# Kernel tuning notes

Hardware: AMD Instinct MI355X
Metric: run time of the kernel (lower is better)

## Reference

```python
import jax, jax.numpy as jnp
import numpy as np

N_STREAMS = 4
N_HEADS = 4
D_STATE = 64
EPS_RMS = float(np.finfo(np.float32).eps)


def rms_norm(x, w):
    v = jnp.mean(x * x, axis=-1, keepdims=True)
    return x * jax.lax.rsqrt(v + EPS_RMS) * w


def sinkhorn_mix(logits, iters=5):
    n = logits.shape[0]
    M = jax.nn.sigmoid(logits) + jnp.eye(n, dtype=logits.dtype)
    for _ in range(iters):
        M = M / (M.sum(axis=1, keepdims=True) + 1e-6)
        M = M / (M.sum(axis=0, keepdims=True) + 1e-6)
    return M


def mamba_block(u, norm_w, Wi, bi, A_log, D, dt_bias, Wo, bo):
    B, L, d_model = u.shape
    d_in = 2 * d_model
    P = d_in // N_HEADS
    un = rms_norm(u, norm_w)
    zxbcdt = un @ Wi + bi  # [B,L,4612]
    z = zxbcdt[:, :, :d_in]
    x = zxbcdt[:, :, d_in:2 * d_in].reshape(B, L, N_HEADS, P)
    dt = zxbcdt[:, :, 2 * d_in:2 * d_in + N_HEADS]
    BC = zxbcdt[:, :, 2 * d_in + N_HEADS:].reshape(B, L, N_HEADS, 2, D_STATE)
    B_mat, C_mat = BC[:, :, :, 0], BC[:, :, :, 1]
    dt = jax.nn.softplus(dt + dt_bias)            # [B,L,H]
    A = -jnp.exp(A_log)                            # [H]
    dtA = jnp.exp(dt * A)                          # [B,L,H]
    dtB = dt[..., None] * B_mat                    # [B,L,H,N]

    # time-major scan over the selective-state recurrence
    def step(h, inp):
        dtA_t, dtB_t, x_t, C_t = inp               # [B,H],[B,H,N],[B,H,P],[B,H,N]
        h = h * dtA_t[:, :, None, None] + dtB_t[..., None] * x_t[:, :, None, :]
        y_t = jnp.einsum('bhn,bhnp->bhp', C_t, h)
        return h, y_t

    h0 = jnp.zeros((B, N_HEADS, D_STATE, P), dtype=u.dtype)
    xs = (jnp.moveaxis(dtA, 1, 0), jnp.moveaxis(dtB, 1, 0),
          jnp.moveaxis(x, 1, 0), jnp.moveaxis(C_mat, 1, 0))
    _, ys = jax.lax.scan(step, h0, xs)             # ys: [L,B,H,P]
    y = jnp.moveaxis(ys, 0, 1)                     # [B,L,H,P]
    y = y + x * D[None, None, :, None]
    y = y.reshape(B, L, d_in) * jax.nn.silu(z)
    return y @ Wo + bo


def setup_inputs() -> dict:
    key = jax.random.key(0)
    ks = jax.random.split(key, 10)
    B, L, d_model, vocab, n_layers = 2, 2048, 1024, 32000, 4
    d_proj_out = 2 * 2 * d_model + 2 * N_HEADS * D_STATE + N_HEADS  # 4612
    d_in = 2 * d_model
    s = lambda f: 1.0 / np.sqrt(f)
    return {
        'tokens': jax.random.randint(ks[0], (B, L), 0, vocab, dtype=jnp.int32),
        'embed': jax.random.normal(ks[1], (vocab, d_model), jnp.float32) * 0.02,
        'norm_w': jnp.ones((n_layers, d_model), jnp.float32),
        'in_proj_W': jax.random.normal(ks[2], (n_layers, d_model, d_proj_out), jnp.float32) * s(d_model),
        'in_proj_b': jnp.zeros((n_layers, d_proj_out), jnp.float32),
        'A_log': jnp.full((n_layers, N_HEADS), -4.0, jnp.float32),
        'D': jnp.ones((n_layers, N_HEADS), jnp.float32),
        'dt_bias': jax.random.uniform(ks[3], (n_layers, N_HEADS), jnp.float32) - 4.0,
        'out_proj_W': jax.random.normal(ks[4], (n_layers, d_in, d_model), jnp.float32) * s(d_in),
        'out_proj_b': jnp.zeros((n_layers, d_model), jnp.float32),
        'mixer_logits': jax.random.normal(ks[5], (n_layers, N_STREAMS, N_STREAMS), jnp.float32) * 0.1,
        'norm_f_w': jnp.ones((d_model,), jnp.float32),
        'head_W': jax.random.normal(ks[6], (d_model, vocab), jnp.float32) * s(d_model),
        'head_b': jnp.zeros((vocab,), jnp.float32),
    }


def reference(tokens, embed, norm_w, in_proj_W, in_proj_b, A_log, D, dt_bias,
              out_proj_W, out_proj_b, mixer_logits, norm_f_w, head_W, head_b):
    B, L = tokens.shape
    d_model = embed.shape[1]
    d_sub = d_model // N_STREAMS
    x = embed[tokens]                              # [B,L,d_model]
    H = x.reshape(B, L, N_STREAMS, d_sub)
    n_layers = norm_w.shape[0]
    for l in range(n_layers):
        M = sinkhorn_mix(mixer_logits[l])
        H_res = jnp.einsum('bsid,ji->bsjd', H, M)
        x_out = mamba_block(H.reshape(B, L, d_model), norm_w[l], in_proj_W[l],
                            in_proj_b[l], A_log[l], D[l], dt_bias[l],
                            out_proj_W[l], out_proj_b[l])
        H = H_res + x_out.reshape(B, L, N_STREAMS, d_sub)
    out = rms_norm(H.reshape(B, L, d_model), norm_f_w)
    return out @ head_W + head_b
```

## Files before the change

kernel.cpp:

```cpp
#include <hip/hip_runtime.h>
#include <hip/hip_fp16.h>
#include <cstdint>


typedef _Float16 f16;
typedef __attribute__((ext_vector_type(8))) _Float16 f16x8;
typedef __attribute__((ext_vector_type(4))) _Float16 f16x4;
typedef __attribute__((ext_vector_type(4))) float f32x4;

#define LDS_CAST(p) ((__attribute__((address_space(3))) void*)(p))
#define GLB_CAST(p) ((const __attribute__((address_space(1))) void*)(p))

static __device__ __forceinline__ void gload16(const void* g, void* l) {
    __builtin_amdgcn_global_load_lds(GLB_CAST(g), LDS_CAST(l), 16, 0, 0);
}

__global__ __launch_bounds__(256) void gemm_f16(
    const f16* __restrict__ A, const f16* __restrict__ Bt,
    const float* __restrict__ bias, float* __restrict__ C,
    int M, int N, int K)
{
    __shared__ f16 As[128 * 32];
    __shared__ f16 Bs[128 * 32];
    const int t = threadIdx.x;
    const int lane = t & 63;
    const int w = t >> 6;

    const int gx = gridDim.x;
    const int gy = gridDim.y;
    const int nwg = gx * gy;
    int lin = blockIdx.y * gx + blockIdx.x;
    int xcd = lin & 7, loc = lin >> 3;
    int q = nwg >> 3, rr = nwg & 7;
    int wg = (xcd < rr) ? (xcd * (q + 1) + loc)
                        : (rr * (q + 1) + (xcd - rr) * q + loc);
    const int GROUP = 8;
    int per_group = GROUP * gy;
    int gid = wg / per_group;
    int first_m = gid * GROUP;
    int gsz = (gx - first_m < GROUP) ? (gx - first_m) : GROUP;
    int inner = wg - gid * per_group;
    const int m0 = (first_m + inner % gsz) * 128;
    const int n0 = (inner / gsz) * 128;

    const int wm0 = (w >> 1) * 64, wn0 = (w & 1) * 64;
    const int mrow = lane & 15, ksel = lane >> 4;

    f32x4 zero = {0.f, 0.f, 0.f, 0.f};
    f32x4 acc[4][4];
#pragma unroll
    for (int i = 0; i < 4; i++)
#pragma unroll
        for (int j = 0; j < 4; j++) acc[i][j] = zero;

    const f16* Abase = A + (size_t)m0 * K;
    const f16* Bbase = Bt + (size_t)n0 * K;

    for (int k0 = 0; k0 < K; k0 += 32) {
#pragma unroll
        for (int i = 0; i < 2; i++) {
            int lin2 = t + i * 256;
            int r = lin2 >> 2;
            int cc = (lin2 & 3) * 8;
            gload16(Abase + (size_t)r * K + k0 + cc, As + lin2 * 8);
            gload16(Bbase + (size_t)r * K + k0 + cc, Bs + lin2 * 8);
        }
        __syncthreads();
        f16x8 af[4], bf[4];
#pragma unroll
        for (int i = 0; i < 4; i++) {
            af[i] = *(const f16x8*)(As + (wm0 + i * 16 + mrow) * 32 + ksel * 8);
            bf[i] = *(const f16x8*)(Bs + (wn0 + i * 16 + mrow) * 32 + ksel * 8);
        }
#pragma unroll
        for (int i = 0; i < 4; i++)
#pragma unroll
            for (int j = 0; j < 4; j++)
                acc[i][j] = __builtin_amdgcn_mfma_f32_16x16x32_f16(bf[j], af[i], acc[i][j], 0, 0, 0);
        __syncthreads();
    }

#pragma unroll
    for (int i = 0; i < 4; i++) {
        int m = m0 + wm0 + i * 16 + mrow;
#pragma unroll
        for (int j = 0; j < 4; j++) {
            int nb = n0 + wn0 + j * 16 + ksel * 4;
            if (nb < N) {
                float4 bv = {0.f, 0.f, 0.f, 0.f};
                if (bias) bv = *(const float4*)(bias + nb);
                float4 v;
                v.x = acc[i][j][0] + bv.x;
                v.y = acc[i][j][1] + bv.y;
                v.z = acc[i][j][2] + bv.z;
                v.w = acc[i][j][3] + bv.w;
                *(float4*)(C + (size_t)m * N + nb) = v;
            }
        }
    }
}

__global__ __launch_bounds__(256) void transpose_w(
    const float* __restrict__ W, f16* __restrict__ Wt, int K, int N, int Npad)
{
    __shared__ float tile[32][33];
    int n0 = blockIdx.x * 32, k0 = blockIdx.y * 32;
    int tx = threadIdx.x & 31, ty = threadIdx.x >> 5;
#pragma unroll
    for (int i = 0; i < 4; i++) {
        int k = k0 + ty + 8 * i;
        int n = n0 + tx;
        tile[ty + 8 * i][tx] = (n < N) ? W[(size_t)k * N + n] : 0.f;
    }
    __syncthreads();
#pragma unroll
    for (int i = 0; i < 4; i++) {
        int n = n0 + ty + 8 * i;
        if (n < Npad) Wt[(size_t)n * K + k0 + tx] = (f16)tile[tx][ty + 8 * i];
    }
}

__global__ void sinkhorn_k(const float* __restrict__ logits, float* __restrict__ Mout)
{
    if (threadIdx.x != 0 || blockIdx.x != 0) return;
    for (int l = 0; l < 4; l++) {
        float M[16];
        for (int i = 0; i < 16; i++) {
            float v = logits[l * 16 + i];
            M[i] = 1.f / (1.f + __expf(-v)) + ((i % 5) == 0 ? 1.f : 0.f);
        }
        for (int it = 0; it < 5; it++) {
            for (int r = 0; r < 4; r++) {
                float s = M[r*4] + M[r*4+1] + M[r*4+2] + M[r*4+3] + 1e-6f;
                for (int c = 0; c < 4; c++) M[r*4+c] /= s;
            }
            for (int c = 0; c < 4; c++) {
                float s = M[c] + M[4+c] + M[8+c] + M[12+c] + 1e-6f;
                for (int r = 0; r < 4; r++) M[r*4+c] /= s;
            }
        }
        for (int i = 0; i < 16; i++) Mout[l * 16 + i] = M[i];
    }
}

__global__ __launch_bounds__(256) void embed_gather(
    const int* __restrict__ tokens, const float* __restrict__ embed, float* __restrict__ H)
{
    int i = blockIdx.x * 256 + threadIdx.x;
    int tok = i >> 8, d4 = i & 255;
    int tk = tokens[tok];
    float4 v = ((const float4*)(embed + (size_t)tk * 1024))[d4];
    ((float4*)(H + (size_t)tok * 1024))[d4] = v;
}

__global__ __launch_bounds__(256) void rmsnorm_k(
    const float* __restrict__ X, const float* __restrict__ w, f16* __restrict__ out)
{
    int tok = blockIdx.x;
    int t = threadIdx.x;
    const float4 v = ((const float4*)(X + (size_t)tok * 1024))[t];
    float ss = v.x*v.x + v.y*v.y + v.z*v.z + v.w*v.w;
#pragma unroll
    for (int off = 32; off > 0; off >>= 1) ss += __shfl_down(ss, off, 64);
    __shared__ float wsum[4];
    if ((t & 63) == 0) wsum[t >> 6] = ss;
    __syncthreads();
    float tot = wsum[0] + wsum[1] + wsum[2] + wsum[3];
    float sc = rsqrtf(tot * (1.f / 1024.f) + 1.1920929e-07f);
    const float4 wv = ((const float4*)w)[t];
    f16x4 o;
    o[0] = (f16)(v.x * sc * wv.x);
    o[1] = (f16)(v.y * sc * wv.y);
    o[2] = (f16)(v.z * sc * wv.z);
    o[3] = (f16)(v.w * sc * wv.w);
    ((f16x4*)(out + (size_t)tok * 1024))[t] = o;
}

__global__ __launch_bounds__(256) void dt_cumsum(
    const float* __restrict__ zx, const float* __restrict__ dt_bias,
    const float* __restrict__ A_log,
    float* __restrict__ dt, float* __restrict__ cum, float* __restrict__ E)
{
    int bh = blockIdx.x;
    int b = bh >> 2, h = bh & 3;
    int t = threadIdx.x;
    float Ah = -__expf(A_log[h]);
    float bias = dt_bias[h];
    float run = 0.f, vals[8];
    for (int i = 0; i < 8; i++) {
        int l = t * 8 + i;
        float raw = zx[((size_t)(b * 2048 + l)) * 4612 + 4096 + h] + bias;
        float dtv = (raw > 20.f) ? raw : log1pf(__expf(raw));
        dt[bh * 2048 + l] = dtv;
        run += dtv * Ah;
        vals[i] = run;
    }
    __shared__ float ps[256];
    ps[t] = run;
    __syncthreads();
    for (int off = 1; off < 256; off <<= 1) {
        float v = (t >= off) ? ps[t - off] : 0.f;
        __syncthreads();
        ps[t] += v;
        __syncthreads();
    }
    float offset = (t > 0) ? ps[t - 1] : 0.f;
    for (int i = 0; i < 8; i++) {
        int l = t * 8 + i;
        float cv = vals[i] + offset;
        cum[bh * 2048 + l] = cv;
        if ((l & 63) == 63) E[bh * 32 + (l >> 6)] = cv;
    }
}

__global__ __launch_bounds__(256) void make_xT(
    const float* __restrict__ zx, f16* __restrict__ xT)
{
    int lb = blockIdx.x * 64, pb = blockIdx.y * 64, bh = blockIdx.z;
    int b = bh >> 2, h = bh & 3;
    __shared__ float tile[64][65];
    int tx = threadIdx.x & 63, ty = threadIdx.x >> 6;
#pragma unroll
    for (int i = 0; i < 16; i++) {
        int ll = ty + 4 * i;
        tile[ll][tx] = zx[((size_t)(b * 2048 + lb + ll)) * 4612 + 2048 + h * 512 + pb + tx];
    }
    __syncthreads();
#pragma unroll
    for (int i = 0; i < 16; i++) {
        int pl = ty + 4 * i;
        xT[((size_t)bh * 512 + pb + pl) * 2048 + lb + tx] = (f16)tile[tx][pl];
    }
}

__global__ __launch_bounds__(256) void make_BC(
    const float* __restrict__ zx, f16* __restrict__ Bc, f16* __restrict__ Cc)
{
    int i = blockIdx.x * 256 + threadIdx.x;
    int n = i & 63, h = (i >> 6) & 3, l = (i >> 8) & 2047, b = i >> 19;
    size_t rowoff = ((size_t)(b * 2048 + l)) * 4612 + 4100 + h * 128;
    size_t o = (((size_t)(b * 4 + h)) * 2048 + l) * 64 + n;
    Bc[o] = (f16)zx[rowoff + n];
    Cc[o] = (f16)zx[rowoff + 64 + n];
}

__global__ __launch_bounds__(256) void chunk_intra(
    const f16* __restrict__ Bc, const f16* __restrict__ Cc,
    const f16* __restrict__ xT,
    const float* __restrict__ dt, const float* __restrict__ cum,
    float* __restrict__ Y, float* __restrict__ Hloc)
{
    int c = blockIdx.x, bh = blockIdx.y;
    int l0 = c * 64;
    __shared__ f16 Cs[4096], Bs2[4096], Sb[4096], Wb[4096];
    __shared__ float cums[64], dts[64];
    int t = threadIdx.x;
    {
        const f16x8* sC = (const f16x8*)(Cc + ((size_t)bh * 2048 + l0) * 64);
        const f16x8* sB = (const f16x8*)(Bc + ((size_t)bh * 2048 + l0) * 64);
        ((f16x8*)Cs)[t] = sC[t];
        ((f16x8*)Cs)[t + 256] = sC[t + 256];
        ((f16x8*)Bs2)[t] = sB[t];
        ((f16x8*)Bs2)[t + 256] = sB[t + 256];
    }
    if (t < 64) {
        cums[t] = cum[bh * 2048 + l0 + t];
        dts[t] = dt[bh * 2048 + l0 + t];
    }
    __syncthreads();
    float cumEnd = cums[63];
    int lane = t & 63, w = t >> 6;
    int mrow = lane & 15, ksel = lane >> 4;

    {
        f16x8 cf[2];
        cf[0] = *(const f16x8*)(Cs + (w * 16 + mrow) * 64 + ksel * 8);
        cf[1] = *(const f16x8*)(Cs + (w * 16 + mrow) * 64 + 32 + ksel * 8);
#pragma unroll
        for (int j = 0; j < 4; j++) {
            f32x4 d = {0.f, 0.f, 0.f, 0.f};
#pragma unroll
            for (int ks = 0; ks < 2; ks++) {
                f16x8 bfv = *(const f16x8*)(Bs2 + (j * 16 + mrow) * 64 + ks * 32 + ksel * 8);
                d = __builtin_amdgcn_mfma_f32_16x16x32_f16(cf[ks], bfv, d, 0, 0, 0);
            }
            int ss = j * 16 + mrow;
#pragma unroll
            for (int r = 0; r < 4; r++) {
                int tt = w * 16 + ksel * 4 + r;
                float sv = (ss <= tt) ? d[r] * __expf(cums[tt] - cums[ss]) * dts[ss] : 0.f;
                Sb[tt * 64 + ss] = (f16)sv;
            }
        }
#pragma unroll
        for (int q2 = 0; q2 < 16; q2++) {
            int idx = t * 16 + q2;
            int tt = idx >> 6, ss = idx & 63;
            float wv = (float)Bs2[ss * 64 + tt] * __expf(cumEnd - cums[ss]) * dts[ss];
            Wb[tt * 64 + ss] = (f16)wv;
        }
    }
    __syncthreads();

    f16x8 sfr[2][4], wfr[2][4];
#pragma unroll
    for (int ks = 0; ks < 2; ks++)
#pragma unroll
        for (int mt = 0; mt < 4; mt++) {
            sfr[ks][mt] = *(const f16x8*)(Sb + (mt * 16 + mrow) * 64 + ks * 32 + ksel * 8);
            wfr[ks][mt] = *(const f16x8*)(Wb + (mt * 16 + mrow) * 64 + ks * 32 + ksel * 8);
        }
    const f16* xbase = xT + ((size_t)bh * 512) * 2048 + c * 64;
    f32x4 zero = {0.f, 0.f, 0.f, 0.f};
#pragma unroll
    for (int ph = 0; ph < 2; ph++) {
        int pb = w * 128 + ph * 64;
        f32x4 aY[4][4], aH[4][4];
#pragma unroll
        for (int i = 0; i < 4; i++)
#pragma unroll
            for (int j = 0; j < 4; j++) { aY[i][j] = zero; aH[i][j] = zero; }
#pragma unroll
        for (int ks = 0; ks < 2; ks++) {
#pragma unroll
            for (int nt = 0; nt < 4; nt++) {
                int pp = pb + nt * 16 + mrow;
                f16x8 bfv = *(const f16x8*)(xbase + (size_t)pp * 2048 + ks * 32 + ksel * 8);
#pragma unroll
                for (int mt = 0; mt < 4; mt++) {
                    aY[mt][nt] = __builtin_amdgcn_mfma_f32_16x16x32_f16(sfr[ks][mt], bfv, aY[mt][nt], 0, 0, 0);
                    aH[mt][nt] = __builtin_amdgcn_mfma_f32_16x16x32_f16(wfr[ks][mt], bfv, aH[mt][nt], 0, 0, 0);
                }
            }
        }
        int r0 = ksel * 4;
#pragma unroll
        for (int mt = 0; mt < 4; mt++)
#pragma unroll
            for (int nt = 0; nt < 4; nt++) {
                int pp = pb + nt * 16 + mrow;
#pragma unroll
                for (int r = 0; r < 4; r++) {
                    int tt = mt * 16 + r0 + r;
                    Y[((size_t)bh * 2048 + l0 + tt) * 512 + pp] = aY[mt][nt][r];
                    Hloc[(((size_t)bh * 32 + c) * 64 + tt) * 512 + pp] = aH[mt][nt][r];
                }
            }
    }
}

__global__ __launch_bounds__(256) void chunk_scan(
    const float* __restrict__ Hloc, const float* __restrict__ E,
    f16* __restrict__ HpreT)
{
    int bh = blockIdx.y;
    int p = blockIdx.x * 64 + (threadIdx.x & 63);
    int nb = blockIdx.z * 16 + (threadIdx.x >> 6) * 4;
    float h[4];
#pragma unroll
    for (int j = 0; j < 4; j++) h[j] = 0.f;
    float Eprev = 0.f;
    for (int c = 0; c < 32; c++) {
        size_t ob = (((size_t)bh * 32 + c) * 512 + p) * 64 + nb;
        f16x4 v;
#pragma unroll
        for (int j = 0; j < 4; j++) v[j] = (f16)h[j];
        *(f16x4*)(HpreT + ob) = v;
        float Ec = E[bh * 32 + c];
        float decay = __expf(Ec - Eprev);
        Eprev = Ec;
        size_t ib = (((size_t)bh * 32 + c) * 64 + nb) * 512 + p;
#pragma unroll
        for (int j = 0; j < 4; j++)
            h[j] = decay * h[j] + Hloc[ib + (size_t)j * 512];
    }
}

__global__ __launch_bounds__(256) void chunk_inter(
    const f16* __restrict__ Cc, const f16* __restrict__ HpreT,
    const float* __restrict__ cum, const float* __restrict__ E,
    const float* __restrict__ Y, const float* __restrict__ zx,
    const float* __restrict__ Dp, f16* __restrict__ ybuf)
{
    int c = blockIdx.x, bh = blockIdx.y;
    int b = bh >> 2, h = bh & 3;
    int l0 = c * 64;
    __shared__ f16 Chat[4096];
    int t = threadIdx.x;
    float Eprev = (c > 0) ? E[bh * 32 + c - 1] : 0.f;
    for (int i = t; i < 4096; i += 256) {
        int tt = i >> 6, n = i & 63;
        float cv = (float)Cc[((size_t)bh * 2048 + l0 + tt) * 64 + n];
        Chat[i] = (f16)(cv * __expf(cum[bh * 2048 + l0 + tt] - Eprev));
    }
    __syncthreads();
    int lane = t & 63, w = t >> 6;
    int mrow = lane & 15, ksel = lane >> 4;
    float Dh = Dp[h];
    f16x8 af[2][4];
#pragma unroll
    for (int ks = 0; ks < 2; ks++)
#pragma unroll
        for (int mt = 0; mt < 4; mt++)
            af[ks][mt] = *(const f16x8*)(Chat + (mt * 16 + mrow) * 64 + ks * 32 + ksel * 8);
    const f16* hb = HpreT + (((size_t)bh * 32 + c) * 512) * 64;
    f32x4 zero = {0.f, 0.f, 0.f, 0.f};
#pragma unroll
    for (int ph = 0; ph < 2; ph++) {
        int pb = w * 128 + ph * 64;
        f32x4 acc[4][4];
#pragma unroll
        for (int i = 0; i < 4; i++)
#pragma unroll
            for (int j = 0; j < 4; j++) acc[i][j] = zero;
#pragma unroll
        for (int ks = 0; ks < 2; ks++) {
#pragma unroll
            for (int nt = 0; nt < 4; nt++) {
                int pp = pb + nt * 16 + mrow;
                f16x8 bfv = *(const f16x8*)(hb + (size_t)pp * 64 + ks * 32 + ksel * 8);
#pragma unroll
                for (int mt = 0; mt < 4; mt++)
                    acc[mt][nt] = __builtin_amdgcn_mfma_f32_16x16x32_f16(af[ks][mt], bfv, acc[mt][nt], 0, 0, 0);
            }
        }
        int r0 = ksel * 4;
#pragma unroll
        for (int mt = 0; mt < 4; mt++)
#pragma unroll
            for (int nt = 0; nt < 4; nt++) {
                int pp = pb + nt * 16 + mrow;
#pragma unroll
                for (int r = 0; r < 4; r++) {
                    int tt = mt * 16 + r0 + r;
                    int l = l0 + tt;
                    size_t zrow = ((size_t)(b * 2048 + l)) * 4612;
                    float y = acc[mt][nt][r] + Y[((size_t)bh * 2048 + l) * 512 + pp];
                    float x = zx[zrow + 2048 + h * 512 + pp];
                    y += x * Dh;
                    float z = zx[zrow + h * 512 + pp];
                    float sig = 1.f / (1.f + __expf(-z));
                    ybuf[((size_t)(b * 2048 + l)) * 2048 + h * 512 + pp] = (f16)(y * z * sig);
                }
            }
    }
}

__global__ __launch_bounds__(256) void mix_add(
    const float* __restrict__ Hold, const float* __restrict__ xout,
    const float* __restrict__ Mm, float* __restrict__ Hnew)
{
    int i = blockIdx.x * 256 + threadIdx.x;
    int j = i & 255, tok = i >> 8;
    size_t rb = (size_t)tok * 1024;
    float h0 = Hold[rb + j], h1 = Hold[rb + 256 + j];
    float h2 = Hold[rb + 512 + j], h3 = Hold[rb + 768 + j];
#pragma unroll
    for (int s = 0; s < 4; s++) {
        float v = Mm[s*4+0]*h0 + Mm[s*4+1]*h1 + Mm[s*4+2]*h2 + Mm[s*4+3]*h3
                + xout[rb + s * 256 + j];
        Hnew[rb + s * 256 + j] = v;
    }
}

extern "C" void kernel_launch(void* const* d_in, const int* in_sizes, int n_in,
                              void* d_out, int out_size, void* d_ws, size_t ws_size,
                              hipStream_t stream)
{
    const int*   tokens     = (const int*)d_in[0];
    const float* embed      = (const float*)d_in[1];
    const float* norm_w     = (const float*)d_in[2];
    const float* in_proj_W  = (const float*)d_in[3];
    const float* in_proj_b  = (const float*)d_in[4];
    const float* A_log      = (const float*)d_in[5];
    const float* Dp         = (const float*)d_in[6];
    const float* dt_bias    = (const float*)d_in[7];
    const float* out_proj_W = (const float*)d_in[8];
    const float* out_proj_b = (const float*)d_in[9];
    const float* mixer_log  = (const float*)d_in[10];
    const float* norm_f_w   = (const float*)d_in[11];
    const float* head_W     = (const float*)d_in[12];
    const float* head_b     = (const float*)d_in[13];
    float* out = (float*)d_out;
    (void)in_sizes; (void)n_in; (void)out_size; (void)ws_size;

    char* base = (char*)d_ws;
    size_t off = 0;
    auto alloc = [&](size_t bytes) -> void* {
        void* r = (void*)(base + off);
        off = (off + bytes + 255) & ~(size_t)255;
        return r;
    };
    f16*   WinT   = (f16*)alloc(4ull * 4736 * 1024 * 2);
    f16*   WoutT  = (f16*)alloc(4ull * 1024 * 2048 * 2);
    f16*   WheadT = (f16*)alloc(32000ull * 1024 * 2);
    float* Mall   = (float*)alloc(64 * 4);
    float* H0     = (float*)alloc(4096ull * 1024 * 4);
    float* H1     = (float*)alloc(4096ull * 1024 * 4);
    f16*   un     = (f16*)alloc(4096ull * 1024 * 2);
    float* zx     = (float*)alloc(4096ull * 4612 * 4);
    float* dtb    = (float*)alloc(8ull * 2048 * 4);
    float* cumb   = (float*)alloc(8ull * 2048 * 4);
    float* Eb     = (float*)alloc(8ull * 32 * 4);
    f16*   xT     = (f16*)alloc(8ull * 512 * 2048 * 2);
    f16*   Bc     = (f16*)alloc(8ull * 2048 * 64 * 2);
    f16*   Cc     = (f16*)alloc(8ull * 2048 * 64 * 2);
    float* Yb     = (float*)alloc(8ull * 2048 * 512 * 4);
    float* Hloc   = (float*)alloc(8ull * 32 * 64 * 512 * 4);
    f16*   HpreT  = (f16*)alloc(8ull * 32 * 512 * 64 * 2);
    f16*   ybuf   = (f16*)alloc(4096ull * 2048 * 2);
    float* xout   = (float*)alloc(4096ull * 1024 * 4);

    for (int l = 0; l < 4; l++) {
        transpose_w<<<dim3(148, 32), 256, 0, stream>>>(
            in_proj_W + (size_t)l * 1024 * 4612, WinT + (size_t)l * 4736 * 1024,
            1024, 4612, 4736);
        transpose_w<<<dim3(32, 64), 256, 0, stream>>>(
            out_proj_W + (size_t)l * 2048 * 1024, WoutT + (size_t)l * 1024 * 2048,
            2048, 1024, 1024);
    }
    transpose_w<<<dim3(1000, 32), 256, 0, stream>>>(head_W, WheadT, 1024, 32000, 32000);
    sinkhorn_k<<<1, 64, 0, stream>>>(mixer_log, Mall);
    embed_gather<<<4096, 256, 0, stream>>>(tokens, embed, H0);

    float* Hc = H0;
    float* Hn = H1;
    for (int l = 0; l < 4; l++) {
        rmsnorm_k<<<4096, 256, 0, stream>>>(Hc, norm_w + l * 1024, un);
        gemm_f16<<<dim3(32, 37), 256, 0, stream>>>(
            un, WinT + (size_t)l * 4736 * 1024, in_proj_b + l * 4612, zx,
            4096, 4612, 1024);
        dt_cumsum<<<8, 256, 0, stream>>>(zx, dt_bias + l * 4, A_log + l * 4, dtb, cumb, Eb);
        make_xT<<<dim3(32, 8, 8), 256, 0, stream>>>(zx, xT);
        make_BC<<<4096, 256, 0, stream>>>(zx, Bc, Cc);
        chunk_intra<<<dim3(32, 8), 256, 0, stream>>>(Bc, Cc, xT, dtb, cumb, Yb, Hloc);
        chunk_scan<<<dim3(8, 8, 4), 256, 0, stream>>>(Hloc, Eb, HpreT);
        chunk_inter<<<dim3(32, 8), 256, 0, stream>>>(Cc, HpreT, cumb, Eb, Yb, zx, Dp + l * 4, ybuf);
        gemm_f16<<<dim3(32, 8), 256, 0, stream>>>(
            ybuf, WoutT + (size_t)l * 1024 * 2048, out_proj_b + l * 1024, xout,
            4096, 1024, 2048);
        mix_add<<<4096, 256, 0, stream>>>(Hc, xout, Mall + l * 16, Hn);
        float* tmp = Hc; Hc = Hn; Hn = tmp;
    }
    rmsnorm_k<<<4096, 256, 0, stream>>>(Hc, norm_f_w, un);
    gemm_f16<<<dim3(32, 250), 256, 0, stream>>>(un, WheadT, head_b, out, 4096, 32000, 1024);
}
```

Before: 2.130 ms.

## Add 256x256-tile triple-buffered GEMM for in-proj and LM head

Introduces a new 512-thread GEMM kernel with 256x256 output tiles, a three-stage LDS ring fed by direct global-to-LDS loads, split A/B prefetch interleaved with MFMA halves, and raised wave priority around MFMA bursts. It replaces the 128x128 GEMM for the in-projection and the large vocab head, aiming for more data reuse per tile and better overlap of loads with compute. The in-proj weight transpose is padded to 4864 columns so N tiles evenly by 256. Larger tiles mean fewer workgroups (304 for the in-projection), which can lower occupancy on 256 CUs and waste work on padded columns.

```diff
diff --git a/kernel.cpp b/kernel.cpp
--- a/kernel.cpp
+++ b/kernel.cpp
@@ -13,6 +13,152 @@
 
 static __device__ __forceinline__ void gload16(const void* g, void* l) {
     __builtin_amdgcn_global_load_lds(GLB_CAST(g), LDS_CAST(l), 16, 0, 0);
+}
+
+__global__ __launch_bounds__(512, 2) void gemm256(
+    const f16* __restrict__ A, const f16* __restrict__ Bt,
+    const float* __restrict__ bias, float* __restrict__ C,
+    int M, int N, int K)
+{
+    __shared__ f16 AS[3 * 256 * 32];
+    __shared__ f16 BS[3 * 256 * 32];
+
+    const int tid = threadIdx.x;
+    const int lane = tid & 63;
+    const int w = tid >> 6;
+    const int wr = w >> 2;
+    const int wc = w & 3;
+    const int mrow = lane & 15, ksel = lane >> 4;
+
+    const int gx = gridDim.x;
+    const int gy = gridDim.y;
+    const int nwg = gx * gy;
+    int lin = blockIdx.y * gx + blockIdx.x;
+    int xcd = lin & 7, loc = lin >> 3;
+    int q = nwg >> 3, rr = nwg & 7;
+    int wg = (xcd < rr) ? (xcd * (q + 1) + loc)
+                        : (rr * (q + 1) + (xcd - rr) * q + loc);
+    const int GROUP = 8;
+    int per_group = GROUP * gy;
+    int gid = wg / per_group;
+    int first_m = gid * GROUP;
+    int gsz = (gx - first_m < GROUP) ? (gx - first_m) : GROUP;
+    int inner = wg - gid * per_group;
+    const int m0 = (first_m + inner % gsz) * 256;
+    const int n0 = (inner / gsz) * 256;
+
+    const int rowt = tid >> 2;
+    const int colE = ((tid & 3) ^ (rowt & 3)) * 8;
+    const int ldst = tid * 8;
+
+    const f16* gA = A + (size_t)m0 * K;
+    const f16* gB = Bt + (size_t)n0 * K;
+    const size_t gofsA0 = (size_t)rowt * K + colE;
+    const size_t gofsA1 = (size_t)(128 + rowt) * K + colE;
+    const size_t gofsB0 = gofsA0;
+    const size_t gofsB1 = gofsA1;
+
+    const int fcol = ((ksel ^ (mrow & 3)) * 8);
+    int offA[8], offB[4];
+#pragma unroll
+    for (int mf = 0; mf < 8; mf++)
+        offA[mf] = (wr * 128 + mf * 16 + mrow) * 32 + fcol;
+#pragma unroll
+    for (int nf = 0; nf < 4; nf++)
+        offB[nf] = (wc * 64 + nf * 16 + mrow) * 32 + fcol;
+
+    f32x4 zero = {0.f, 0.f, 0.f, 0.f};
+    f32x4 acc[8][4];
+#pragma unroll
+    for (int i = 0; i < 8; i++)
+#pragma unroll
+        for (int j = 0; j < 4; j++) acc[i][j] = zero;
+
+    const int nt = K >> 5;
+
+#pragma unroll
+    for (int T = 0; T < 2; ++T) {
+        gload16(gA + gofsA0 + (size_t)T * 32, AS + T * 8192 + ldst);
+        gload16(gA + gofsA1 + (size_t)T * 32, AS + T * 8192 + 4096 + ldst);
+        gload16(gB + gofsB0 + (size_t)T * 32, BS + T * 8192 + ldst);
+        gload16(gB + gofsB1 + (size_t)T * 32, BS + T * 8192 + 4096 + ldst);
+    }
+    asm volatile("s_waitcnt vmcnt(4)" ::: "memory");
+    __builtin_amdgcn_sched_barrier(0);
+    __builtin_amdgcn_s_barrier();
+
+    for (int t = 0; t < nt; ++t) {
+        const int slot = t % 3;
+        const f16* as = AS + slot * 8192;
+        const f16* bs = BS + slot * 8192;
+        const int sst = (t + 2) % 3;
+        const bool st = (t + 2) < nt;
+        const size_t kof = (size_t)(t + 2) * 32;
+
+        f16x8 af[4], bf[4];
+#pragma unroll
+        for (int mf = 0; mf < 4; mf++) af[mf] = *(const f16x8*)(as + offA[mf]);
+#pragma unroll
+        for (int nf = 0; nf < 4; nf++) bf[nf] = *(const f16x8*)(bs + offB[nf]);
+        if (st) {
+            gload16(gA + gofsA0 + kof, AS + sst * 8192 + ldst);
+            gload16(gA + gofsA1 + kof, AS + sst * 8192 + 4096 + ldst);
+        }
+        __builtin_amdgcn_s_barrier();
+        __builtin_amdgcn_s_setprio(1);
+#pragma unroll
+        for (int mf = 0; mf < 4; mf++)
+#pragma unroll
+            for (int nf = 0; nf < 4; nf++)
+                acc[mf][nf] = __builtin_amdgcn_mfma_f32_16x16x32_f16(bf[nf], af[mf], acc[mf][nf], 0, 0, 0);
+        __builtin_amdgcn_s_setprio(0);
+        __builtin_amdgcn_s_barrier();
+
+        f16x8 af2[4];
+#pragma unroll
+        for (int mf = 0; mf < 4; mf++) af2[mf] = *(const f16x8*)(as + offA[4 + mf]);
+        if (st) {
+            gload16(gB + gofsB0 + kof, BS + sst * 8192 + ldst);
+            gload16(gB + gofsB1 + kof, BS + sst * 8192 + 4096 + ldst);
+        }
+        __builtin_amdgcn_s_barrier();
+        __builtin_amdgcn_s_setprio(1);
+#pragma unroll
+        for (int mf = 0; mf < 4; mf++)
+#pragma unroll
+            for (int nf = 0; nf < 4; nf++)
+                acc[4 + mf][nf] = __builtin_amdgcn_mfma_f32_16x16x32_f16(bf[nf], af2[mf], acc[4 + mf][nf], 0, 0, 0);
+        __builtin_amdgcn_s_setprio(0);
+
+        if (t + 1 < nt) {
+            if (st) {
+                asm volatile("s_waitcnt vmcnt(4)" ::: "memory");
+            } else {
+                asm volatile("s_waitcnt vmcnt(0)" ::: "memory");
+            }
+            __builtin_amdgcn_sched_barrier(0);
+            __builtin_amdgcn_s_barrier();
+        }
+    }
+
+#pragma unroll
+    for (int mf = 0; mf < 8; mf++) {
+        int m = m0 + wr * 128 + mf * 16 + mrow;
+#pragma unroll
+        for (int nf = 0; nf < 4; nf++) {
+            int nb = n0 + wc * 64 + nf * 16 + ksel * 4;
+            if (nb < N) {
+                float4 bv = {0.f, 0.f, 0.f, 0.f};
+                if (bias) bv = *(const float4*)(bias + nb);
+                float4 v;
+                v.x = acc[mf][nf][0] + bv.x;
+                v.y = acc[mf][nf][1] + bv.y;
+                v.z = acc[mf][nf][2] + bv.z;
+                v.w = acc[mf][nf][3] + bv.w;
+                *(float4*)(C + (size_t)m * N + nb) = v;
+            }
+        }
+    }
 }
 
 __global__ __launch_bounds__(256) void gemm_f16(
@@ -491,7 +637,7 @@
         off = (off + bytes + 255) & ~(size_t)255;
         return r;
     };
-    f16*   WinT   = (f16*)alloc(4ull * 4736 * 1024 * 2);
+    f16*   WinT   = (f16*)alloc(4ull * 4864 * 1024 * 2);
     f16*   WoutT  = (f16*)alloc(4ull * 1024 * 2048 * 2);
     f16*   WheadT = (f16*)alloc(32000ull * 1024 * 2);
     float* Mall   = (float*)alloc(64 * 4);
@@ -512,9 +658,9 @@
     float* xout   = (float*)alloc(4096ull * 1024 * 4);
 
     for (int l = 0; l < 4; l++) {
-        transpose_w<<<dim3(148, 32), 256, 0, stream>>>(
-            in_proj_W + (size_t)l * 1024 * 4612, WinT + (size_t)l * 4736 * 1024,
-            1024, 4612, 4736);
+        transpose_w<<<dim3(152, 32), 256, 0, stream>>>(
+            in_proj_W + (size_t)l * 1024 * 4612, WinT + (size_t)l * 4864 * 1024,
+            1024, 4612, 4864);
         transpose_w<<<dim3(32, 64), 256, 0, stream>>>(
             out_proj_W + (size_t)l * 2048 * 1024, WoutT + (size_t)l * 1024 * 2048,
             2048, 1024, 1024);
@@ -527,8 +673,8 @@
     float* Hn = H1;
     for (int l = 0; l < 4; l++) {
         rmsnorm_k<<<4096, 256, 0, stream>>>(Hc, norm_w + l * 1024, un);
-        gemm_f16<<<dim3(32, 37), 256, 0, stream>>>(
-            un, WinT + (size_t)l * 4736 * 1024, in_proj_b + l * 4612, zx,
+        gemm256<<<dim3(16, 19), 512, 0, stream>>>(
+            un, WinT + (size_t)l * 4864 * 1024, in_proj_b + l * 4612, zx,
             4096, 4612, 1024);
         dt_cumsum<<<8, 256, 0, stream>>>(zx, dt_bias + l * 4, A_log + l * 4, dtb, cumb, Eb);
         make_xT<<<dim3(32, 8, 8), 256, 0, stream>>>(zx, xT);
@@ -543,5 +689,5 @@
         float* tmp = Hc; Hc = Hn; Hn = tmp;
     }
     rmsnorm_k<<<4096, 256, 0, stream>>>(Hc, norm_f_w, un);
-    gemm_f16<<<dim3(32, 250), 256, 0, stream>>>(un, WheadT, head_b, out, 4096, 32000, 1024);
-}
+    gemm256<<<dim3(16, 125), 512, 0, stream>>>(un, WheadT, head_b, out, 4096, 32000, 1024);
+}
```

Result: no change. 2.100 ms (-1.4%).
